# Kernel optimization log

Hardware: AMD Instinct MI355X
Metric: run time of the kernel (lower is better)

The kernel has to match this reference:

```python
import jax, jax.numpy as jnp
import numpy as np

NUM_HEADS = 16

def setup_inputs() -> dict:
    key = jax.random.key(0)
    ks = jax.random.split(key, 8)
    T, B, E = 2048, 2, 1024
    s = 1.0 / np.sqrt(E)
    return {
        "query": jax.random.normal(ks[0], (T, B, E), jnp.float32),
        "key": jax.random.normal(ks[1], (T, B, E), jnp.float32),
        "value": jax.random.normal(ks[2], (T, B, E), jnp.float32),
        "Wq": jax.random.normal(ks[3], (E, E), jnp.float32) * s,
        "bq": jnp.zeros((E,), jnp.float32),
        "Wk": jax.random.normal(ks[4], (E, E), jnp.float32) * s,
        "bk": jnp.zeros((E,), jnp.float32),
        "Wv": jax.random.normal(ks[5], (E, E), jnp.float32) * s,
        "bv": jnp.zeros((E,), jnp.float32),
        "Wo": jax.random.normal(ks[6], (E, E), jnp.float32) * s,
        "bo": jnp.zeros((E,), jnp.float32),
    }

def reference(query, key, value, Wq, bq, Wk, bk, Wv, bv, Wo, bo):
    T, B, E = query.shape
    S = key.shape[0]
    H = NUM_HEADS
    hd = E // H
    scaling = float(hd) ** -0.5
    # linear projections (torch Linear: x @ W.T + b)
    q = (query @ Wq.T + bq).reshape(T, B, H, hd)
    k = (key @ Wk.T + bk).reshape(S, B, H, hd)
    v = (value @ Wv.T + bv).reshape(S, B, H, hd)
    # scores: (B, H, T, S)
    scores = jnp.einsum('tbhd,sbhd->bhts', q, k) * scaling
    attn = jax.nn.softmax(scores, axis=-1)  # dropout p=0
    # weighted sum: (T, B, H, hd) -> (T, B, E)
    out = jnp.einsum('bhts,sbhd->tbhd', attn, v).reshape(T, B, E)
    out = out @ Wo.T + bo
    # averaged attention weights over heads: (B, T, S)
    avg_w = attn.mean(axis=1)
    return (out, avg_w)
```

## Files before the change

### kernel.cpp

```cpp
#include <hip/hip_runtime.h>
#include <hip/hip_bf16.h>
#include <stdint.h>

#define HN 16
#define TT 2048
#define BBATCH 2
#define EE 1024
#define HD 64
#define MM 4096

#define SCALEQ 0.18033688011112042f

typedef __attribute__((ext_vector_type(8))) __bf16 bfrag;
typedef __attribute__((ext_vector_type(4))) float f32x4;
typedef __attribute__((ext_vector_type(4))) short s16x4;

__device__ __forceinline__ void gll16(const void* g, void* lds) {
  __builtin_amdgcn_global_load_lds(
      (const __attribute__((address_space(1))) void*)g,
      (__attribute__((address_space(3))) void*)lds, 16, 0, 0);
}

__device__ __forceinline__ f32x4 mfma_bf16(bfrag a, bfrag b, f32x4 c) {
  return __builtin_amdgcn_mfma_f32_16x16x32_bf16(a, b, c, 0, 0, 0);
}

__device__ __forceinline__ const bfrag* fragp(const __bf16* base, int row, int e) {
  return (const bfrag*)(base + row * 64 + ((((e >> 3) ^ row) & 7) << 3));
}
__device__ __forceinline__ void stage8(const __bf16* grow0, int gstride,
                                       __bf16* tile, int r0, int lane) {
  const int rr = lane >> 3;
  const int cl = (lane & 7) ^ rr;
  gll16(grow0 + (size_t)(r0 + rr) * gstride + cl * 8, tile + r0 * 64);
}

struct CvtArgs {
  const float* src[7];
  __bf16* dst[7];
  int n4[7];
};

__global__ __launch_bounds__(256) void cvt_all(CvtArgs a) {
  const int z = blockIdx.z;
  const int i = blockIdx.x * 256 + threadIdx.x;
  if (i < a.n4[z]) {
    float4 v = ((const float4*)a.src[z])[i];
    struct alignas(8) B4 { __bf16 a0, a1, a2, a3; };
    B4 o = {(__bf16)v.x, (__bf16)v.y, (__bf16)v.z, (__bf16)v.w};
    ((B4*)a.dst[z])[i] = o;
  }
}

__device__ __forceinline__ void gemm_core(const __bf16* __restrict__ X,
                                          const __bf16* __restrict__ W,
                                          const float* __restrict__ bias,
                                          void* __restrict__ out, int mode,
                                          float scale) {
  __shared__ __bf16 As[128 * 32];
  __shared__ __bf16 Bs[128 * 32];
  const int tid = threadIdx.x;
  const int lane = tid & 63, wave = tid >> 6;
  const int wm = wave >> 1, wn = wave & 1;
  const int quad = lane >> 4, l16 = lane & 15;
  const int m0 = blockIdx.y * 128, n0 = blockIdx.x * 128;
  const int srow = lane >> 2;
  const int scol = (lane & 3) * 8;
  const int c0 = 2 * wave;

  f32x4 acc[4][4] = {};

  for (int k0 = 0; k0 < EE; k0 += 32) {
    #pragma unroll
    for (int c = 0; c < 2; ++c) {
      const int ch = c0 + c;
      gll16(X + (size_t)(m0 + ch * 16 + srow) * EE + k0 + scol, As + ch * 512);
      gll16(W + (size_t)(n0 + ch * 16 + srow) * EE + k0 + scol, Bs + ch * 512);
    }
    __syncthreads();
    bfrag a[4], b[4];
    #pragma unroll
    for (int f = 0; f < 4; ++f)
      a[f] = *(const bfrag*)(As + (wm * 64 + f * 16 + l16) * 32 + quad * 8);
    #pragma unroll
    for (int f = 0; f < 4; ++f)
      b[f] = *(const bfrag*)(Bs + (wn * 64 + f * 16 + l16) * 32 + quad * 8);
    #pragma unroll
    for (int fm = 0; fm < 4; ++fm)
      #pragma unroll
      for (int fn = 0; fn < 4; ++fn)
        acc[fm][fn] = mfma_bf16(a[fm], b[fn], acc[fm][fn]);
    __syncthreads();
  }

  float bv[4];
  #pragma unroll
  for (int fn = 0; fn < 4; ++fn) bv[fn] = bias[n0 + wn * 64 + fn * 16 + l16];

  #pragma unroll
  for (int fm = 0; fm < 4; ++fm) {
    #pragma unroll
    for (int r = 0; r < 4; ++r) {
      const int gm = m0 + wm * 64 + fm * 16 + quad * 4 + r;
      #pragma unroll
      for (int fn = 0; fn < 4; ++fn) {
        const int gn = n0 + wn * 64 + fn * 16 + l16;
        const float v = (acc[fm][fn][r] + bv[fn]) * scale;
        if (mode == 0) {
          const int t = gm >> 1, bb = gm & 1, h = gn >> 6, d = gn & 63;
          ((__bf16*)out)[(((size_t)(bb * HN + h)) * TT + t) * HD + d] = (__bf16)v;
        } else {
          const int s = gm >> 1, bb = gm & 1, h = gn >> 6, d = gn & 63;
          ((__bf16*)out)[(((size_t)(bb * HN + h)) * HD + d) * TT + s] = (__bf16)v;
        }
      }
    }
  }
}

__global__ __launch_bounds__(256) void gemm_qkv(
    const __bf16* __restrict__ xq, const __bf16* __restrict__ xk,
    const __bf16* __restrict__ xv, const __bf16* __restrict__ wq,
    const __bf16* __restrict__ wk, const __bf16* __restrict__ wv,
    const float* __restrict__ bq, const float* __restrict__ bk,
    const float* __restrict__ bv, __bf16* __restrict__ qo,
    __bf16* __restrict__ ko, __bf16* __restrict__ vo) {
  const __bf16 *X, *W;
  const float* bias;
  __bf16* out;
  int mode;
  float scale;
  if (blockIdx.z == 0)      { X = xq; W = wq; bias = bq; out = qo; mode = 0; scale = SCALEQ; }
  else if (blockIdx.z == 1) { X = xk; W = wk; bias = bk; out = ko; mode = 0; scale = 1.0f; }
  else                      { X = xv; W = wv; bias = bv; out = vo; mode = 2; scale = 1.0f; }
  gemm_core(X, W, bias, out, mode, scale);
}

__global__ __launch_bounds__(256) void gemm_o64(const __bf16* __restrict__ X,
                                                const __bf16* __restrict__ W,
                                                const float* __restrict__ bias,
                                                float* __restrict__ out) {
  __shared__ __bf16 As[64 * 32];
  __shared__ __bf16 Bs[128 * 32];
  const int tid = threadIdx.x;
  const int lane = tid & 63, wave = tid >> 6;
  const int quad = lane >> 4, l16 = lane & 15;
  const int m0 = blockIdx.y * 64, n0 = blockIdx.x * 128;
  const int srow = lane >> 2, scol = (lane & 3) * 8;

  f32x4 acc[4][2] = {};

  for (int k0 = 0; k0 < EE; k0 += 32) {
    gll16(X + (size_t)(m0 + wave * 16 + srow) * EE + k0 + scol, As + wave * 512);
    #pragma unroll
    for (int c = 0; c < 2; ++c) {
      const int ch = 2 * wave + c;
      gll16(W + (size_t)(n0 + ch * 16 + srow) * EE + k0 + scol, Bs + ch * 512);
    }
    __syncthreads();
    bfrag a[4], b2[2];
    #pragma unroll
    for (int f = 0; f < 4; ++f)
      a[f] = *(const bfrag*)(As + (f * 16 + l16) * 32 + quad * 8);
    #pragma unroll
    for (int f = 0; f < 2; ++f)
      b2[f] = *(const bfrag*)(Bs + (wave * 32 + f * 16 + l16) * 32 + quad * 8);
    #pragma unroll
    for (int fm = 0; fm < 4; ++fm)
      #pragma unroll
      for (int fn = 0; fn < 2; ++fn)
        acc[fm][fn] = mfma_bf16(a[fm], b2[fn], acc[fm][fn]);
    __syncthreads();
  }

  float bv[2];
  #pragma unroll
  for (int fn = 0; fn < 2; ++fn) bv[fn] = bias[n0 + wave * 32 + fn * 16 + l16];

  #pragma unroll
  for (int fm = 0; fm < 4; ++fm)
    #pragma unroll
    for (int r = 0; r < 4; ++r) {
      const int gm = m0 + fm * 16 + quad * 4 + r;
      #pragma unroll
      for (int fn = 0; fn < 2; ++fn) {
        const int gn = n0 + wave * 32 + fn * 16 + l16;
        out[(size_t)gm * EE + gn] = acc[fm][fn][r] + bv[fn];
      }
    }
}

__global__ __launch_bounds__(256, 2) void attn_fwd(const __bf16* __restrict__ qb,
                                                   const __bf16* __restrict__ kb,
                                                   const __bf16* __restrict__ vtb,
                                                   __bf16* __restrict__ ob,
                                                   float* __restrict__ linv_ws) {
  union Sh {
    __bf16 kv[2][2][2][64 * 64];
    float om[2][64 * 64];
  };
  __shared__ Sh sm;
  __shared__ float Lsum[2][128];
  __shared__ float LinvS[128];

  const int tid = threadIdx.x, lane = tid & 63, w = tid >> 6;
  const int p = w >> 1, tw = w & 1;
  const int quad = lane >> 4, l16 = lane & 15;

  const int bx = blockIdx.x;
  const int xcd = bx & 7, slot = bx >> 3;
  const int bhi = xcd * 4 + (slot >> 4);
  const int t0 = (slot & 15) * 128;
  const int b = bhi >> 4, h = bhi & 15;
  const size_t bh = (size_t)(b * HN + h);

  const __bf16* qbase = qb + (bh * TT + t0) * HD;
  const __bf16* kbase = kb + bh * TT * HD;
  const __bf16* vbase = vtb + bh * HD * TT;
  const int sBase = p * 1024;

  #pragma unroll
  for (int c = 0; c < 4; ++c) {
    stage8(kbase + (size_t)sBase * HD, HD, sm.kv[p][0][0], tw * 32 + c * 8, lane);
    stage8(vbase + sBase, TT, sm.kv[p][1][0], tw * 32 + c * 8, lane);
  }

  bfrag qf[4][2];
  #pragma unroll
  for (int fn = 0; fn < 4; ++fn)
    #pragma unroll
    for (int ks = 0; ks < 2; ++ks)
      qf[fn][ks] = *(const bfrag*)(qbase +
          (size_t)(tw * 64 + fn * 16 + l16) * HD + ks * 32 + quad * 8);

  f32x4 oacc[4][4] = {};
  float lpart[4] = {};

  for (int it = 0; it < 16; ++it) {
    const int cur = it & 1;
    __syncthreads();
    if (it + 1 < 16) {
      const int s1 = sBase + (it + 1) * 64;
      #pragma unroll
      for (int c = 0; c < 4; ++c) {
        stage8(kbase + (size_t)s1 * HD, HD, sm.kv[p][0][1 - cur], tw * 32 + c * 8, lane);
        stage8(vbase + s1, TT, sm.kv[p][1][1 - cur], tw * 32 + c * 8, lane);
      }
    }

    f32x4 sacc[4][4] = {};
    #pragma unroll
    for (int ks = 0; ks < 2; ++ks) {
      bfrag kf[4];
      #pragma unroll
      for (int fm = 0; fm < 4; ++fm)
        kf[fm] = *fragp(sm.kv[p][0][cur], fm * 16 + l16, ks * 32 + quad * 8);
      #pragma unroll
      for (int fm = 0; fm < 4; ++fm)
        #pragma unroll
        for (int fn = 0; fn < 4; ++fn)
          sacc[fm][fn] = mfma_bf16(kf[fm], qf[fn][ks], sacc[fm][fn]);
    }

    union PB { __bf16 hh[8]; bfrag v; } pb[2][4];
    #pragma unroll
    for (int fm = 0; fm < 4; ++fm)
      #pragma unroll
      for (int fn = 0; fn < 4; ++fn) {
        const float p0 = __builtin_amdgcn_exp2f(sacc[fm][fn][0]);
        const float p1 = __builtin_amdgcn_exp2f(sacc[fm][fn][1]);
        const float p2 = __builtin_amdgcn_exp2f(sacc[fm][fn][2]);
        const float p3 = __builtin_amdgcn_exp2f(sacc[fm][fn][3]);
        lpart[fn] += (p0 + p1) + (p2 + p3);
        const int hb = (fm & 1) * 4;
        pb[fm >> 1][fn].hh[hb + 0] = (__bf16)p0;
        pb[fm >> 1][fn].hh[hb + 1] = (__bf16)p1;
        pb[fm >> 1][fn].hh[hb + 2] = (__bf16)p2;
        pb[fm >> 1][fn].hh[hb + 3] = (__bf16)p3;
      }

    #pragma unroll
    for (int ks = 0; ks < 2; ++ks) {
      bfrag vf[4];
      #pragma unroll
      for (int fm = 0; fm < 4; ++fm) {
        const __bf16* base = sm.kv[p][1][cur] + (fm * 16 + l16) * 64;
        const int sw = l16 & 7, qh = quad >> 1, qo = (quad & 1) * 4;
        union VF { s16x4 q[2]; bfrag v; } u;
        u.q[0] = *(const s16x4*)(base + (((ks * 4 + qh) ^ sw) << 3) + qo);
        u.q[1] = *(const s16x4*)(base + (((ks * 4 + 2 + qh) ^ sw) << 3) + qo);
        vf[fm] = u.v;
      }
      #pragma unroll
      for (int fm = 0; fm < 4; ++fm)
        #pragma unroll
        for (int fn = 0; fn < 4; ++fn)
          oacc[fm][fn] = mfma_bf16(vf[fm], pb[ks][fn].v, oacc[fm][fn]);
    }
  }

  #pragma unroll
  for (int fn = 0; fn < 4; ++fn) {
    float v = lpart[fn];
    v += __shfl_xor(v, 16);
    v += __shfl_xor(v, 32);
    lpart[fn] = v;
  }
  if (quad == 0)
    #pragma unroll
    for (int fn = 0; fn < 4; ++fn)
      Lsum[p][tw * 64 + fn * 16 + l16] = lpart[fn];

  __syncthreads();

  if (p == 1) {
    #pragma unroll
    for (int fm = 0; fm < 4; ++fm)
      #pragma unroll
      for (int fn = 0; fn < 4; ++fn)
        #pragma unroll
        for (int r = 0; r < 4; ++r)
          sm.om[tw][(fm * 16 + quad * 4 + r) * 64 + fn * 16 + l16] = oacc[fm][fn][r];
  }
  if (tid < 128) {
    const float linv = 1.0f / (Lsum[0][tid] + Lsum[1][tid]);
    LinvS[tid] = linv;
    linv_ws[bh * TT + t0 + tid] = linv;
  }
  __syncthreads();

  if (p == 0) {
    float li[4];
    #pragma unroll
    for (int fn = 0; fn < 4; ++fn) li[fn] = LinvS[tw * 64 + fn * 16 + l16];
    #pragma unroll
    for (int fm = 0; fm < 4; ++fm)
      #pragma unroll
      for (int fn = 0; fn < 4; ++fn) {
        const int t = t0 + tw * 64 + fn * 16 + l16;
        struct alignas(8) B4 { __bf16 a0, a1, a2, a3; };
        B4 o;
        __bf16* op = &o.a0;
        #pragma unroll
        for (int r = 0; r < 4; ++r) {
          const float v = (oacc[fm][fn][r] +
              sm.om[tw][(fm * 16 + quad * 4 + r) * 64 + fn * 16 + l16]) * li[fn];
          op[r] = (__bf16)v;
        }
        *(B4*)(ob + ((size_t)t * BBATCH + b) * EE + h * HD + fm * 16 + quad * 4) = o;
      }
  }
}

__global__ __launch_bounds__(256, 2) void avg_attn(const __bf16* __restrict__ qb,
                                                   const __bf16* __restrict__ kb,
                                                   const float* __restrict__ linv_ws,
                                                   float* __restrict__ avg_out) {
  __shared__ __bf16 Qs[2][128 * 64];
  __shared__ __bf16 Ks[2][128 * 64];

  const int tid = threadIdx.x, lane = tid & 63, w = tid >> 6;
  const int wm = w >> 1, wn = w & 1;
  const int quad = lane >> 4, l16 = lane & 15;

  const int bx = blockIdx.x;
  const int xcd = bx & 7, slot = bx >> 3;
  const int bti = xcd * 4 + (slot >> 4);
  const int s0 = (slot & 15) * 128;
  const int b = bti >> 4, t0 = (bti & 15) * 128;

  const __bf16* qt = qb + (((size_t)b * HN) * TT + t0) * HD;
  const __bf16* kt = kb + (((size_t)b * HN) * TT + s0) * HD;
  const float* lrow0 = linv_ws + ((size_t)b * HN) * TT + t0 + wm * 64;

  #pragma unroll
  for (int c = 0; c < 4; ++c) {
    stage8(qt, HD, Qs[0], w * 32 + c * 8, lane);
    stage8(kt, HD, Ks[0], w * 32 + c * 8, lane);
  }

  f32x4 aacc[4][4] = {};

  for (int h = 0; h < HN; ++h) {
    const int cur = h & 1;
    __syncthreads();
    if (h + 1 < HN) {
      const __bf16* qn = qt + (size_t)(h + 1) * TT * HD;
      const __bf16* kn = kt + (size_t)(h + 1) * TT * HD;
      #pragma unroll
      for (int c = 0; c < 4; ++c) {
        stage8(qn, HD, Qs[1 - cur], w * 32 + c * 8, lane);
        stage8(kn, HD, Ks[1 - cur], w * 32 + c * 8, lane);
      }
    }

    f32x4 sacc[4][4] = {};
    #pragma unroll
    for (int ks = 0; ks < 2; ++ks) {
      bfrag qf4[4], kf4[4];
      #pragma unroll
      for (int f = 0; f < 4; ++f)
        qf4[f] = *fragp(Qs[cur], wm * 64 + f * 16 + l16, ks * 32 + quad * 8);
      #pragma unroll
      for (int f = 0; f < 4; ++f)
        kf4[f] = *fragp(Ks[cur], wn * 64 + f * 16 + l16, ks * 32 + quad * 8);
      #pragma unroll
      for (int fm = 0; fm < 4; ++fm)
        #pragma unroll
        for (int fn = 0; fn < 4; ++fn)
          sacc[fm][fn] = mfma_bf16(qf4[fm], kf4[fn], sacc[fm][fn]);
    }

    const float* lr = lrow0 + (size_t)h * TT;
    f32x4 lvv[4];
    #pragma unroll
    for (int fm = 0; fm < 4; ++fm)
      lvv[fm] = *(const f32x4*)(lr + fm * 16 + quad * 4);

    #pragma unroll
    for (int fm = 0; fm < 4; ++fm)
      #pragma unroll
      for (int fn = 0; fn < 4; ++fn)
        #pragma unroll
        for (int r = 0; r < 4; ++r)
          aacc[fm][fn][r] += __builtin_amdgcn_exp2f(sacc[fm][fn][r]) * lvv[fm][r];
  }

  const float invh = 1.0f / (float)HN;
  #pragma unroll
  for (int fm = 0; fm < 4; ++fm)
    #pragma unroll
    for (int r = 0; r < 4; ++r) {
      const int t = t0 + wm * 64 + fm * 16 + quad * 4 + r;
      #pragma unroll
      for (int fn = 0; fn < 4; ++fn) {
        const int s = s0 + wn * 64 + fn * 16 + l16;
        avg_out[((size_t)b * TT + t) * TT + s] = aacc[fm][fn][r] * invh;
      }
    }
}

extern "C" void kernel_launch(void* const* d_in, const int* in_sizes, int n_in,
                              void* d_out, int out_size, void* d_ws, size_t ws_size,
                              hipStream_t stream) {
  (void)in_sizes; (void)n_in; (void)out_size; (void)ws_size;
  const float* query = (const float*)d_in[0];
  const float* key   = (const float*)d_in[1];
  const float* value = (const float*)d_in[2];
  const float* Wq = (const float*)d_in[3];
  const float* bq = (const float*)d_in[4];
  const float* Wk = (const float*)d_in[5];
  const float* bk = (const float*)d_in[6];
  const float* Wv = (const float*)d_in[7];
  const float* bv = (const float*)d_in[8];
  const float* Wo = (const float*)d_in[9];
  const float* bo = (const float*)d_in[10];

  char* ws = (char*)d_ws;
  size_t off = 0;
  auto wsalloc = [&](size_t bytes) -> void* {
    void* p = ws + off;
    off += (bytes + 255) & ~(size_t)255;
    return p;
  };
  const size_t XE = (size_t)MM * EE;
  const size_t WE = (size_t)EE * EE;
  __bf16* xq   = (__bf16*)wsalloc(XE * 2);
  __bf16* xk   = (__bf16*)wsalloc(XE * 2);
  __bf16* xv   = (__bf16*)wsalloc(XE * 2);
  __bf16* wqb  = (__bf16*)wsalloc(WE * 2);
  __bf16* wkb  = (__bf16*)wsalloc(WE * 2);
  __bf16* wvb  = (__bf16*)wsalloc(WE * 2);
  __bf16* wob  = (__bf16*)wsalloc(WE * 2);
  __bf16* qbuf = (__bf16*)wsalloc(XE * 2);
  __bf16* kbuf = (__bf16*)wsalloc(XE * 2);
  __bf16* vtbuf= (__bf16*)wsalloc(XE * 2);
  __bf16* obuf = (__bf16*)wsalloc(XE * 2);
  float* linv  = (float*)wsalloc((size_t)BBATCH * HN * TT * 4);

  CvtArgs ca;
  ca.src[0] = query; ca.dst[0] = xq;  ca.n4[0] = (int)(XE / 4);
  ca.src[1] = key;   ca.dst[1] = xk;  ca.n4[1] = (int)(XE / 4);
  ca.src[2] = value; ca.dst[2] = xv;  ca.n4[2] = (int)(XE / 4);
  ca.src[3] = Wq;    ca.dst[3] = wqb; ca.n4[3] = (int)(WE / 4);
  ca.src[4] = Wk;    ca.dst[4] = wkb; ca.n4[4] = (int)(WE / 4);
  ca.src[5] = Wv;    ca.dst[5] = wvb; ca.n4[5] = (int)(WE / 4);
  ca.src[6] = Wo;    ca.dst[6] = wob; ca.n4[6] = (int)(WE / 4);
  cvt_all<<<dim3(4096, 1, 7), 256, 0, stream>>>(ca);

  gemm_qkv<<<dim3(8, 32, 3), 256, 0, stream>>>(xq, xk, xv, wqb, wkb, wvb,
                                               bq, bk, bv, qbuf, kbuf, vtbuf);

  attn_fwd<<<dim3(512), 256, 0, stream>>>(qbuf, kbuf, vtbuf, obuf, linv);

  float* avg_out = (float*)d_out + (size_t)TT * BBATCH * EE;
  avg_attn<<<dim3(512), 256, 0, stream>>>(qbuf, kbuf, linv, avg_out);

  gemm_o64<<<dim3(8, 64), 256, 0, stream>>>(obuf, wob, bo, (float*)d_out);
}
```

Baseline: 264.7 us.

## Double-buffer GEMM K-loop with 64-wide K tiles and unified templated GEMM

Replaces the single-buffered 32-wide K loop in the QKV and output projection GEMMs with a double-buffered 64-wide K loop. The next tile's global-to-LDS staging is issued before the MFMAs on the current tile, and one of the two barriers per iteration is removed. The output GEMM now shares the templated core, and both kernels use 1D grids with a 2-blocks-per-CU launch bound. The cost is more LDS per block (up to 64KB), which may limit occupancy, and the change relies on stage8/fragp helpers that sit in the hidden lines.

```diff
diff --git a/kernel.cpp b/kernel.cpp
--- a/kernel.cpp
+++ b/kernel.cpp
@@ -52,45 +52,56 @@
   }
 }
 
-__device__ __forceinline__ void gemm_core(const __bf16* __restrict__ X,
-                                          const __bf16* __restrict__ W,
-                                          const float* __restrict__ bias,
-                                          void* __restrict__ out, int mode,
-                                          float scale) {
-  __shared__ __bf16 As[128 * 32];
-  __shared__ __bf16 Bs[128 * 32];
-  const int tid = threadIdx.x;
-  const int lane = tid & 63, wave = tid >> 6;
-  const int wm = wave >> 1, wn = wave & 1;
+template <int MT>
+__device__ __forceinline__ void gemm2(const __bf16* __restrict__ X,
+                                      const __bf16* __restrict__ W,
+                                      const float* __restrict__ bias,
+                                      void* __restrict__ out, int mode,
+                                      float scale, int m0, int n0,
+                                      __bf16* As0, __bf16* As1,
+                                      __bf16* Bs0, __bf16* Bs1) {
+  const int tid = threadIdx.x, lane = tid & 63, w = tid >> 6;
+  const int wm = w >> 1, wn = w & 1;
   const int quad = lane >> 4, l16 = lane & 15;
-  const int m0 = blockIdx.y * 128, n0 = blockIdx.x * 128;
-  const int srow = lane >> 2;
-  const int scol = (lane & 3) * 8;
-  const int c0 = 2 * wave;
-
-  f32x4 acc[4][4] = {};
-
-  for (int k0 = 0; k0 < EE; k0 += 32) {
-    #pragma unroll
-    for (int c = 0; c < 2; ++c) {
-      const int ch = c0 + c;
-      gll16(X + (size_t)(m0 + ch * 16 + srow) * EE + k0 + scol, As + ch * 512);
-      gll16(W + (size_t)(n0 + ch * 16 + srow) * EE + k0 + scol, Bs + ch * 512);
-    }
+  constexpr int FM = MT / 32;
+
+  auto stageAB = [&](int buf, int k0) {
+    __bf16* A = buf ? As1 : As0;
+    __bf16* B = buf ? Bs1 : Bs0;
+    #pragma unroll
+    for (int c = 0; c < FM; ++c)
+      stage8(X + (size_t)m0 * EE + k0, EE, A, w * (MT / 4) + c * 8, lane);
+    #pragma unroll
+    for (int c = 0; c < 4; ++c)
+      stage8(W + (size_t)n0 * EE + k0, EE, B, w * 32 + c * 8, lane);
+  };
+
+  stageAB(0, 0);
+
+  f32x4 acc[FM][4] = {};
+
+  for (int it = 0; it < EE / 64; ++it) {
+    const int cur = it & 1;
     __syncthreads();
-    bfrag a[4], b[4];
-    #pragma unroll
-    for (int f = 0; f < 4; ++f)
-      a[f] = *(const bfrag*)(As + (wm * 64 + f * 16 + l16) * 32 + quad * 8);
-    #pragma unroll
-    for (int f = 0; f < 4; ++f)
-      b[f] = *(const bfrag*)(Bs + (wn * 64 + f * 16 + l16) * 32 + quad * 8);
-    #pragma unroll
-    for (int fm = 0; fm < 4; ++fm)
-      #pragma unroll
-      for (int fn = 0; fn < 4; ++fn)
-        acc[fm][fn] = mfma_bf16(a[fm], b[fn], acc[fm][fn]);
-    __syncthreads();
+    if (it + 1 < EE / 64) stageAB(1 - cur, (it + 1) * 64);
+
+    const __bf16* A = cur ? As1 : As0;
+    const __bf16* B = cur ? Bs1 : Bs0;
+    #pragma unroll
+    for (int ks = 0; ks < 2; ++ks) {
+      bfrag a[FM], b[4];
+      #pragma unroll
+      for (int f = 0; f < FM; ++f)
+        a[f] = *fragp(A, wm * (MT / 2) + f * 16 + l16, ks * 32 + quad * 8);
+      #pragma unroll
+      for (int f = 0; f < 4; ++f)
+        b[f] = *fragp(B, wn * 64 + f * 16 + l16, ks * 32 + quad * 8);
+      #pragma unroll
+      for (int fm = 0; fm < FM; ++fm)
+        #pragma unroll
+        for (int fn = 0; fn < 4; ++fn)
+          acc[fm][fn] = mfma_bf16(a[fm], b[fn], acc[fm][fn]);
+    }
   }
 
   float bv[4];
@@ -98,10 +109,10 @@
   for (int fn = 0; fn < 4; ++fn) bv[fn] = bias[n0 + wn * 64 + fn * 16 + l16];
 
   #pragma unroll
-  for (int fm = 0; fm < 4; ++fm) {
+  for (int fm = 0; fm < FM; ++fm) {
     #pragma unroll
     for (int r = 0; r < 4; ++r) {
-      const int gm = m0 + wm * 64 + fm * 16 + quad * 4 + r;
+      const int gm = m0 + wm * (MT / 2) + fm * 16 + quad * 4 + r;
       #pragma unroll
       for (int fn = 0; fn < 4; ++fn) {
         const int gn = n0 + wn * 64 + fn * 16 + l16;
@@ -109,85 +120,50 @@
         if (mode == 0) {
           const int t = gm >> 1, bb = gm & 1, h = gn >> 6, d = gn & 63;
           ((__bf16*)out)[(((size_t)(bb * HN + h)) * TT + t) * HD + d] = (__bf16)v;
-        } else {
+        } else if (mode == 2) {
           const int s = gm >> 1, bb = gm & 1, h = gn >> 6, d = gn & 63;
           ((__bf16*)out)[(((size_t)(bb * HN + h)) * HD + d) * TT + s] = (__bf16)v;
+        } else {
+          ((float*)out)[(size_t)gm * EE + gn] = v;
         }
       }
     }
   }
 }
 
-__global__ __launch_bounds__(256) void gemm_qkv(
+__global__ __launch_bounds__(256, 2) void gemm_qkv(
     const __bf16* __restrict__ xq, const __bf16* __restrict__ xk,
     const __bf16* __restrict__ xv, const __bf16* __restrict__ wq,
     const __bf16* __restrict__ wk, const __bf16* __restrict__ wv,
     const float* __restrict__ bq, const float* __restrict__ bk,
     const float* __restrict__ bv, __bf16* __restrict__ qo,
     __bf16* __restrict__ ko, __bf16* __restrict__ vo) {
+  __shared__ __bf16 As[2][128 * 64];
+  __shared__ __bf16 Bs[2][128 * 64];
+  const int bx = blockIdx.x;
+  const int m = bx & 31, n = (bx >> 5) & 7, z = bx >> 8;
   const __bf16 *X, *W;
   const float* bias;
   __bf16* out;
   int mode;
   float scale;
-  if (blockIdx.z == 0)      { X = xq; W = wq; bias = bq; out = qo; mode = 0; scale = SCALEQ; }
-  else if (blockIdx.z == 1) { X = xk; W = wk; bias = bk; out = ko; mode = 0; scale = 1.0f; }
-  else                      { X = xv; W = wv; bias = bv; out = vo; mode = 2; scale = 1.0f; }
-  gemm_core(X, W, bias, out, mode, scale);
-}
-
-__global__ __launch_bounds__(256) void gemm_o64(const __bf16* __restrict__ X,
-                                                const __bf16* __restrict__ W,
-                                                const float* __restrict__ bias,
-                                                float* __restrict__ out) {
-  __shared__ __bf16 As[64 * 32];
-  __shared__ __bf16 Bs[128 * 32];
-  const int tid = threadIdx.x;
-  const int lane = tid & 63, wave = tid >> 6;
-  const int quad = lane >> 4, l16 = lane & 15;
-  const int m0 = blockIdx.y * 64, n0 = blockIdx.x * 128;
-  const int srow = lane >> 2, scol = (lane & 3) * 8;
-
-  f32x4 acc[4][2] = {};
-
-  for (int k0 = 0; k0 < EE; k0 += 32) {
-    gll16(X + (size_t)(m0 + wave * 16 + srow) * EE + k0 + scol, As + wave * 512);
-    #pragma unroll
-    for (int c = 0; c < 2; ++c) {
-      const int ch = 2 * wave + c;
-      gll16(W + (size_t)(n0 + ch * 16 + srow) * EE + k0 + scol, Bs + ch * 512);
-    }
-    __syncthreads();
-    bfrag a[4], b2[2];
-    #pragma unroll
-    for (int f = 0; f < 4; ++f)
-      a[f] = *(const bfrag*)(As + (f * 16 + l16) * 32 + quad * 8);
-    #pragma unroll
-    for (int f = 0; f < 2; ++f)
-      b2[f] = *(const bfrag*)(Bs + (wave * 32 + f * 16 + l16) * 32 + quad * 8);
-    #pragma unroll
-    for (int fm = 0; fm < 4; ++fm)
-      #pragma unroll
-      for (int fn = 0; fn < 2; ++fn)
-        acc[fm][fn] = mfma_bf16(a[fm], b2[fn], acc[fm][fn]);
-    __syncthreads();
-  }
-
-  float bv[2];
-  #pragma unroll
-  for (int fn = 0; fn < 2; ++fn) bv[fn] = bias[n0 + wave * 32 + fn * 16 + l16];
-
-  #pragma unroll
-  for (int fm = 0; fm < 4; ++fm)
-    #pragma unroll
-    for (int r = 0; r < 4; ++r) {
-      const int gm = m0 + fm * 16 + quad * 4 + r;
-      #pragma unroll
-      for (int fn = 0; fn < 2; ++fn) {
-        const int gn = n0 + wave * 32 + fn * 16 + l16;
-        out[(size_t)gm * EE + gn] = acc[fm][fn][r] + bv[fn];
-      }
-    }
+  if (z == 0)      { X = xq; W = wq; bias = bq; out = qo; mode = 0; scale = SCALEQ; }
+  else if (z == 1) { X = xk; W = wk; bias = bk; out = ko; mode = 0; scale = 1.0f; }
+  else             { X = xv; W = wv; bias = bv; out = vo; mode = 2; scale = 1.0f; }
+  gemm2<128>(X, W, bias, out, mode, scale, m * 128, n * 128,
+             As[0], As[1], Bs[0], Bs[1]);
+}
+
+__global__ __launch_bounds__(256, 2) void gemm_o(const __bf16* __restrict__ X,
+                                                 const __bf16* __restrict__ W,
+                                                 const float* __restrict__ bias,
+                                                 float* __restrict__ out) {
+  __shared__ __bf16 As[2][64 * 64];
+  __shared__ __bf16 Bs[2][128 * 64];
+  const int bx = blockIdx.x;
+  const int m = bx & 63, n = bx >> 6;
+  gemm2<64>(X, W, bias, out, 3, 1.0f, m * 64, n * 128,
+            As[0], As[1], Bs[0], Bs[1]);
 }
 
 __global__ __launch_bounds__(256, 2) void attn_fwd(const __bf16* __restrict__ qb,
@@ -488,13 +464,13 @@
   ca.src[6] = Wo;    ca.dst[6] = wob; ca.n4[6] = (int)(WE / 4);
   cvt_all<<<dim3(4096, 1, 7), 256, 0, stream>>>(ca);
 
-  gemm_qkv<<<dim3(8, 32, 3), 256, 0, stream>>>(xq, xk, xv, wqb, wkb, wvb,
-                                               bq, bk, bv, qbuf, kbuf, vtbuf);
+  gemm_qkv<<<dim3(768), 256, 0, stream>>>(xq, xk, xv, wqb, wkb, wvb,
+                                          bq, bk, bv, qbuf, kbuf, vtbuf);
 
   attn_fwd<<<dim3(512), 256, 0, stream>>>(qbuf, kbuf, vtbuf, obuf, linv);
 
   float* avg_out = (float*)d_out + (size_t)TT * BBATCH * EE;
   avg_attn<<<dim3(512), 256, 0, stream>>>(qbuf, kbuf, linv, avg_out);
 
-  gemm_o64<<<dim3(8, 64), 256, 0, stream>>>(obuf, wob, bo, (float*)d_out);
-}
+  gemm_o<<<dim3(512), 256, 0, stream>>>(obuf, wob, bo, (float*)d_out);
+}
```

After: 247.4 us. 6.5% less time.
